# Performance work log

Hardware: AMD Instinct MI355X
Metric: run time of the kernel (lower is better)

Reference implementation:

```python
import jax, jax.numpy as jnp
import numpy as np

N, C = 1048576, 27

def setup_inputs() -> dict:
    key = jax.random.key(0)
    k1, k2, k3 = jax.random.split(key, 3)
    predicted = jax.random.normal(k1, (N, C), dtype=jnp.float32)
    target = jax.random.uniform(k2, (N, C), dtype=jnp.float32)
    # penalty matrix normally loaded from CSV; values in (0, 1] after normalization
    penalty = jax.random.uniform(k3, (C, C), dtype=jnp.float32)
    penalty = penalty / penalty.max()
    return {"predicted": predicted, "target": target, "penalty": penalty}

def reference(predicted, target, penalty):
    # per-row L1 sum: [N]
    raw_l1 = jnp.sum(jnp.abs(predicted - target), axis=-1)
    # per-row argmax indices for prediction and label classes: [N]
    pred_cls = jnp.argmax(predicted, axis=-1)
    label_cls = jnp.argmax(target, axis=-1)
    # gather penalty[pred_cls, label_cls]: [N]
    pen = penalty[pred_cls, label_cls]
    return jnp.sum(raw_l1 * pen) / predicted.shape[0]
```

## Files before the change

### kernel.cpp

```cpp
#include <hip/hip_runtime.h>

#define NROWS 1048576
#define NCLS 27
#define RPB 256
#define NBLK (NROWS / RPB)

__global__ __launch_bounds__(256) void l1pen_partial(
    const float* __restrict__ pred, const float* __restrict__ tgt,
    const float* __restrict__ pen, float* __restrict__ partial) {
  __shared__ float sp[RPB * NCLS];
  __shared__ float st[RPB * NCLS];
  __shared__ float spen[NCLS * NCLS];
  __shared__ float sred[4];
  const int tid = threadIdx.x;

  for (int i = tid; i < NCLS * NCLS; i += 256) spen[i] = pen[i];

  const size_t base = (size_t)blockIdx.x * (RPB * NCLS);
  const float4* p4 = (const float4*)(pred + base);
  const float4* t4 = (const float4*)(tgt + base);
  float4* sp4 = (float4*)sp;
  float4* st4 = (float4*)st;
  constexpr int NV4 = RPB * NCLS / 4;
  #pragma unroll
  for (int i = 0; i < NV4 / 256; ++i) {
    sp4[tid + i * 256] = p4[tid + i * 256];
    st4[tid + i * 256] = t4[tid + i * 256];
  }
  {
    const int i = tid + (NV4 / 256) * 256;
    if (i < NV4) { sp4[i] = p4[i]; st4[i] = t4[i]; }
  }
  __syncthreads();

  const float* rp = sp + tid * NCLS;
  const float* rt = st + tid * NCLS;
  float p0 = rp[0], t0 = rt[0];
  float l1 = fabsf(p0 - t0);
  float pbest = p0, tbest = t0;
  int pc = 0, lc = 0;
  #pragma unroll
  for (int c = 1; c < NCLS; ++c) {
    float p = rp[c], t = rt[c];
    l1 += fabsf(p - t);
    if (p > pbest) { pbest = p; pc = c; }
    if (t > tbest) { tbest = t; lc = c; }
  }
  float val = l1 * spen[pc * NCLS + lc];

  #pragma unroll
  for (int off = 32; off; off >>= 1) val += __shfl_down(val, off);
  if ((tid & 63) == 0) sred[tid >> 6] = val;
  __syncthreads();
  if (tid == 0)
    partial[blockIdx.x] = (sred[0] + sred[1]) + (sred[2] + sred[3]);
}

__global__ __launch_bounds__(256) void l1pen_final(
    const float* __restrict__ partial, float* __restrict__ out) {
  __shared__ double sred[4];
  double s = 0.0;
  for (int i = threadIdx.x; i < NBLK; i += 256) s += (double)partial[i];
  #pragma unroll
  for (int off = 32; off; off >>= 1) s += __shfl_down(s, off);
  if ((threadIdx.x & 63) == 0) sred[threadIdx.x >> 6] = s;
  __syncthreads();
  if (threadIdx.x == 0)
    out[0] = (float)(((sred[0] + sred[1]) + (sred[2] + sred[3])) / (double)NROWS);
}

extern "C" void kernel_launch(void* const* d_in, const int* in_sizes, int n_in,
                              void* d_out, int out_size, void* d_ws, size_t ws_size,
                              hipStream_t stream) {
  const float* pred = (const float*)d_in[0];
  const float* tgt  = (const float*)d_in[1];
  const float* pen  = (const float*)d_in[2];
  float* out        = (float*)d_out;
  float* partial    = (float*)d_ws;

  l1pen_partial<<<NBLK, 256, 0, stream>>>(pred, tgt, pen, partial);
  l1pen_final<<<1, 256, 0, stream>>>(partial, out);
}
```

Baseline: 44.90 us.

## Split each row across two threads and halve rows per block

Each row's 27 classes are now split between a pair of threads (14 and 13 columns). The partial L1 sums and argmax results are merged with xor shuffles, using tie-breaking on the lower index. Rows per block drop to 128, which halves the LDS footprint and doubles the block count, and a minimum of 5 blocks per CU is requested in launch bounds. The aim is more occupancy and more memory-level parallelism on a bandwidth-bound reduction, at the cost of extra shuffles and more partials to reduce at the end.

After: 49.45 us. +10.1%, slower.

```diff
diff --git a/kernel.cpp b/kernel.cpp
--- a/kernel.cpp
+++ b/kernel.cpp
@@ -2,10 +2,10 @@
 
 #define NROWS 1048576
 #define NCLS 27
-#define RPB 256
+#define RPB 128
 #define NBLK (NROWS / RPB)
 
-__global__ __launch_bounds__(256) void l1pen_partial(
+__global__ __launch_bounds__(256, 5) void l1pen_partial(
     const float* __restrict__ pred, const float* __restrict__ tgt,
     const float* __restrict__ pen, float* __restrict__ partial) {
   __shared__ float sp[RPB * NCLS];
@@ -23,30 +23,51 @@
   float4* st4 = (float4*)st;
   constexpr int NV4 = RPB * NCLS / 4;
   #pragma unroll
-  for (int i = 0; i < NV4 / 256; ++i) {
+  for (int i = 0; i < 3; ++i) {
     sp4[tid + i * 256] = p4[tid + i * 256];
     st4[tid + i * 256] = t4[tid + i * 256];
   }
-  {
-    const int i = tid + (NV4 / 256) * 256;
-    if (i < NV4) { sp4[i] = p4[i]; st4[i] = t4[i]; }
+  if (tid < NV4 - 768) {
+    sp4[tid + 768] = p4[tid + 768];
+    st4[tid + 768] = t4[tid + 768];
   }
   __syncthreads();
 
-  const float* rp = sp + tid * NCLS;
-  const float* rt = st + tid * NCLS;
+  const int row = tid >> 1;
+  const int half = tid & 1;
+  const int cbase = half ? 14 : 0;
+  const float* rp = sp + row * NCLS + cbase;
+  const float* rt = st + row * NCLS + cbase;
+
   float p0 = rp[0], t0 = rt[0];
   float l1 = fabsf(p0 - t0);
   float pbest = p0, tbest = t0;
   int pc = 0, lc = 0;
   #pragma unroll
-  for (int c = 1; c < NCLS; ++c) {
-    float p = rp[c], t = rt[c];
+  for (int j = 1; j < 13; ++j) {
+    float p = rp[j], t = rt[j];
     l1 += fabsf(p - t);
-    if (p > pbest) { pbest = p; pc = c; }
-    if (t > tbest) { tbest = t; lc = c; }
+    if (p > pbest) { pbest = p; pc = j; }
+    if (t > tbest) { tbest = t; lc = j; }
   }
-  float val = l1 * spen[pc * NCLS + lc];
+  if (!half) {
+    float p = rp[13], t = rt[13];
+    l1 += fabsf(p - t);
+    if (p > pbest) { pbest = p; pc = 13; }
+    if (t > tbest) { tbest = t; lc = 13; }
+  }
+  pc += cbase; lc += cbase;
+
+  float l1o = __shfl_xor(l1, 1);
+  float pbo = __shfl_xor(pbest, 1);
+  int   pco = __shfl_xor(pc, 1);
+  float tbo = __shfl_xor(tbest, 1);
+  int   lco = __shfl_xor(lc, 1);
+  l1 += l1o;
+  if (pbo > pbest || (pbo == pbest && pco < pc)) { pbest = pbo; pc = pco; }
+  if (tbo > tbest || (tbo == tbest && lco < lc)) { tbest = tbo; lc = lco; }
+
+  float val = half ? 0.0f : l1 * spen[pc * NCLS + lc];
 
   #pragma unroll
   for (int off = 32; off; off >>= 1) val += __shfl_down(val, off);
```

## Double-buffer row tiles via async global-to-LDS loads in persistent blocks

Applied to the files above, without the earlier changes.

Each block now loops over several 64-row tiles and uses a fixed grid of 2048 blocks. Tiles are staged with global_load_lds direct-to-LDS copies into two buffers, so the next tile loads while the current one is processed. Each row is split across four threads, which merge their L1 sums and argmax results with shuffles. The aim is to overlap memory traffic with compute and cut register-staged copies. The cost is a barrier per tile, and correctness depends on the barrier waiting for the async LDS loads to finish.

After: 45.51 us. About the same (+1.4%).

```diff
diff --git a/kernel.cpp b/kernel.cpp
--- a/kernel.cpp
+++ b/kernel.cpp
@@ -2,55 +2,95 @@
 
 #define NROWS 1048576
 #define NCLS 27
-#define RPB 256
-#define NBLK (NROWS / RPB)
+#define TROWS 64
+#define TELEM (TROWS * NCLS)
+#define TV4 (TELEM / 4)
+#define NTILES (NROWS / TROWS)
+#define GRID 2048
+#define TPB (NTILES / GRID)
+
+typedef __attribute__((address_space(3))) void       lds_vp;
+typedef __attribute__((address_space(1))) const void glb_vp;
+
+__device__ __forceinline__ void glds16(const float4* g, float4* l) {
+  __builtin_amdgcn_global_load_lds((glb_vp*)g, (lds_vp*)l, 16, 0, 0);
+}
+
+__device__ __forceinline__ void stage_tile(
+    const float* pred, const float* tgt, float4 (*sbuf4)[2][TV4],
+    int b, int tile, int tid) {
+  const float4* p4 = (const float4*)pred + (size_t)tile * TV4;
+  const float4* t4 = (const float4*)tgt  + (size_t)tile * TV4;
+  glds16(&p4[tid], &sbuf4[b][0][tid]);
+  glds16(&t4[tid], &sbuf4[b][1][tid]);
+  if (tid < TV4 - 256) {
+    glds16(&p4[256 + tid], &sbuf4[b][0][256 + tid]);
+    glds16(&t4[256 + tid], &sbuf4[b][1][256 + tid]);
+  }
+}
 
 __global__ __launch_bounds__(256) void l1pen_partial(
     const float* __restrict__ pred, const float* __restrict__ tgt,
     const float* __restrict__ pen, float* __restrict__ partial) {
-  __shared__ float sp[RPB * NCLS];
-  __shared__ float st[RPB * NCLS];
+  __shared__ float4 sbuf4[2][2][TV4];
   __shared__ float spen[NCLS * NCLS];
   __shared__ float sred[4];
   const int tid = threadIdx.x;
 
   for (int i = tid; i < NCLS * NCLS; i += 256) spen[i] = pen[i];
 
-  const size_t base = (size_t)blockIdx.x * (RPB * NCLS);
-  const float4* p4 = (const float4*)(pred + base);
-  const float4* t4 = (const float4*)(tgt + base);
-  float4* sp4 = (float4*)sp;
-  float4* st4 = (float4*)st;
-  constexpr int NV4 = RPB * NCLS / 4;
-  #pragma unroll
-  for (int i = 0; i < NV4 / 256; ++i) {
-    sp4[tid + i * 256] = p4[tid + i * 256];
-    st4[tid + i * 256] = t4[tid + i * 256];
-  }
-  {
-    const int i = tid + (NV4 / 256) * 256;
-    if (i < NV4) { sp4[i] = p4[i]; st4[i] = t4[i]; }
-  }
+  const int tile0 = blockIdx.x * TPB;
+  stage_tile(pred, tgt, sbuf4, 0, tile0, tid);
   __syncthreads();
 
-  const float* rp = sp + tid * NCLS;
-  const float* rt = st + tid * NCLS;
-  float p0 = rp[0], t0 = rt[0];
-  float l1 = fabsf(p0 - t0);
-  float pbest = p0, tbest = t0;
-  int pc = 0, lc = 0;
-  #pragma unroll
-  for (int c = 1; c < NCLS; ++c) {
-    float p = rp[c], t = rt[c];
-    l1 += fabsf(p - t);
-    if (p > pbest) { pbest = p; pc = c; }
-    if (t > tbest) { tbest = t; lc = c; }
+  const int q = tid & 3;
+  const int r = tid >> 2;
+  const int cbase = q * 7;
+  float acc = 0.f;
+
+  for (int t = 0; t < TPB; ++t) {
+    const int cur = t & 1;
+    if (t + 1 < TPB)
+      stage_tile(pred, tgt, sbuf4, cur ^ 1, tile0 + t + 1, tid);
+
+    const float* sp = (const float*)&sbuf4[cur][0][0];
+    const float* st = (const float*)&sbuf4[cur][1][0];
+    const float* rp = sp + r * NCLS + cbase;
+    const float* rt = st + r * NCLS + cbase;
+
+    float p0 = rp[0], t0 = rt[0];
+    float l1 = fabsf(p0 - t0);
+    float pb = p0, tb = t0;
+    int pc = cbase, lc = cbase;
+    #pragma unroll
+    for (int j = 1; j < 7; ++j) {
+      if (cbase + j < NCLS) {
+        float p = rp[j], tt = rt[j];
+        l1 += fabsf(p - tt);
+        if (p > pb)  { pb = p;  pc = cbase + j; }
+        if (tt > tb) { tb = tt; lc = cbase + j; }
+      }
+    }
+
+    #pragma unroll
+    for (int m = 1; m <= 2; m <<= 1) {
+      float l1o = __shfl_xor(l1, m);
+      float pbo = __shfl_xor(pb, m); int pco = __shfl_xor(pc, m);
+      float tbo = __shfl_xor(tb, m); int lco = __shfl_xor(lc, m);
+      l1 += l1o;
+      if (pbo > pb || (pbo == pb && pco < pc)) { pb = pbo; pc = pco; }
+      if (tbo > tb || (tbo == tb && lco < lc)) { tb = tbo; lc = lco; }
+    }
+
+    float pe = spen[pc * NCLS + lc];
+    acc += (q == 0) ? l1 * pe : 0.f;
+
+    __syncthreads();
   }
-  float val = l1 * spen[pc * NCLS + lc];
 
   #pragma unroll
-  for (int off = 32; off; off >>= 1) val += __shfl_down(val, off);
-  if ((tid & 63) == 0) sred[tid >> 6] = val;
+  for (int off = 32; off; off >>= 1) acc += __shfl_down(acc, off);
+  if ((tid & 63) == 0) sred[tid >> 6] = acc;
   __syncthreads();
   if (tid == 0)
     partial[blockIdx.x] = (sred[0] + sred[1]) + (sred[2] + sred[3]);
@@ -60,7 +100,7 @@
     const float* __restrict__ partial, float* __restrict__ out) {
   __shared__ double sred[4];
   double s = 0.0;
-  for (int i = threadIdx.x; i < NBLK; i += 256) s += (double)partial[i];
+  for (int i = threadIdx.x; i < GRID; i += 256) s += (double)partial[i];
   #pragma unroll
   for (int off = 32; off; off >>= 1) s += __shfl_down(s, off);
   if ((threadIdx.x & 63) == 0) sred[threadIdx.x >> 6] = s;
@@ -78,6 +118,6 @@
   float* out        = (float*)d_out;
   float* partial    = (float*)d_ws;
 
-  l1pen_partial<<<NBLK, 256, 0, stream>>>(pred, tgt, pen, partial);
+  l1pen_partial<<<GRID, 256, 0, stream>>>(pred, tgt, pen, partial);
   l1pen_final<<<1, 256, 0, stream>>>(partial, out);
 }
```
